# Kernel optimization log

Hardware: AMD Instinct MI355X
Metric: run time of the kernel (lower is better)

## Reference

```python
import jax, jax.numpy as jnp
import numpy as np

N, E, U, L = 10000, 320000, 256, 3


def setup_inputs() -> dict:
    key = jax.random.key(0)
    ks = jax.random.split(key, 16)
    s = 0.05
    p = {}
    p["pos"] = jax.random.normal(ks[0], (N, 2), jnp.float32)
    p["edge_attr_in"] = jax.random.uniform(ks[1], (E, 1), jnp.float32)
    p["edge_index"] = jax.random.randint(ks[2], (2, E), 0, N)
    p["Wp"] = jax.random.normal(ks[3], (2, U), jnp.float32) * s
    p["bp"] = jnp.zeros((U,), jnp.float32)
    p["Wa"] = jax.random.normal(ks[4], (1, U), jnp.float32) * s
    p["ba"] = jnp.zeros((U,), jnp.float32)
    p["W1"] = jax.random.normal(ks[5], (L, U, U), jnp.float32) * s
    p["b1"] = jnp.zeros((L, U), jnp.float32)
    p["W2"] = jax.random.normal(ks[6], (L, U, U), jnp.float32) * s
    p["b2"] = jnp.zeros((L, U), jnp.float32)
    p["We"] = jax.random.normal(ks[7], (L + 1, U, U), jnp.float32) * s
    p["be"] = jnp.zeros((L + 1, U), jnp.float32)
    p["Ws"] = jax.random.normal(ks[8], (L + 1, U, U), jnp.float32) * s
    p["Wt"] = jax.random.normal(ks[9], (L + 1, U, U), jnp.float32) * s
    p["Wm1"] = jax.random.normal(ks[10], (U + 1, U // 2), jnp.float32) * s
    p["bm1"] = jnp.zeros((U // 2,), jnp.float32)
    p["alpha"] = 0.25 * jnp.ones((1,), jnp.float32)  # PReLU default slope
    p["Wm2"] = jax.random.normal(ks[11], (U // 2, 1), jnp.float32) * s
    p["bm2"] = jnp.zeros((1,), jnp.float32)
    return p


def _forward(pos, edge_attr_in, edge_index, Wp, bp, Wa, ba, W1, b1, W2, b2,
             We, be, Ws, Wt, Wm1, bm1, alpha, Wm2, bm2):
    src, dst = edge_index[0], edge_index[1]
    x = pos @ Wp + bp                      # [N, U]
    e = edge_attr_in @ Wa + ba             # [E, U]

    def edge_update(x, e, l):
        # ResEdgeLinear: residual edge update from endpoint nodes + edge feats
        return e + jax.nn.relu(e @ We[l] + x[src] @ Ws[l] + x[dst] @ Wt[l] + be[l])

    for l in range(L):
        # ResNodeConv: gated gather-linear-scatter with residual
        gate = jax.nn.sigmoid(e)                                   # [E, U]
        msg = gate * (x[src] @ W2[l] + b2[l])                      # [E, U]
        agg = jax.ops.segment_sum(msg, dst, num_segments=N)        # [N, U]
        x_new = x + jax.nn.relu(x @ W1[l] + b1[l] + agg)
        e_new = edge_update(x, e, l)  # simultaneous update: both use old (x, e)
        x, e = x_new, e_new
    e = edge_update(x, e, L)

    h = jnp.concatenate([e, edge_attr_in[:, :1]], axis=-1) @ Wm1 + bm1
    h = jnp.where(h > 0, h, alpha * h)  # PReLU
    return h @ Wm2 + bm2                # [E, 1] logits


def reference(pos, edge_attr_in, edge_index, Wp, bp, Wa, ba, W1, b1, W2, b2,
              We, be, Ws, Wt, Wm1, bm1, alpha, Wm2, bm2):
    return _forward(pos, edge_attr_in, edge_index, Wp, bp, Wa, ba, W1, b1,
                    W2, b2, We, be, Ws, Wt, Wm1, bm1, alpha, Wm2, bm2)
```

## Files before the change

### kernel.cpp

```cpp
#include <hip/hip_runtime.h>
#include <stdint.h>

#define N_NODES 10000
#define N_EDGES 320000

using bf16x8 = __attribute__((ext_vector_type(8))) short;
using fp32x4 = __attribute__((ext_vector_type(4))) float;
using u16x8 = __attribute__((ext_vector_type(8))) unsigned short;
using i32x4 = __attribute__((ext_vector_type(4))) int;

__device__ __forceinline__ float bf2f(unsigned short u) {
  union { unsigned int i; float f; } v; v.i = ((unsigned int)u) << 16; return v.f;
}
__device__ __forceinline__ unsigned short f2bf(float f) {
  union { float f; unsigned int i; } v; v.f = f;
  unsigned int x = v.i;
  x += 0x7fffu + ((x >> 16) & 1u);
  return (unsigned short)(x >> 16);
}

#define A_POS 0
#define A_EA 20000
#define A_WP 340000
#define A_BP 340512
#define A_WA 340768
#define A_BA 341024
#define A_W1 341280
#define A_B1 537888
#define A_W2 538656
#define A_B2 735264
#define A_WE 736032
#define A_BE 998176
#define A_WS 999200
#define A_WT 1261344
#define A_WM1 1523488
#define A_BM1 1556384
#define A_AL 1556512
#define A_WM2 1556544
#define A_BM2 1556672
#define ARENA_USED 1556673
#define ARENA_TOT 1556736

__constant__ int g_off[19] = {A_POS, A_EA, A_WP, A_BP, A_WA, A_BA, A_W1, A_B1,
                              A_W2, A_B2, A_WE, A_BE, A_WS, A_WT, A_WM1,
                              A_BM1, A_AL, A_WM2, A_BM2};

struct Ptrs { const void* p[19]; };

__global__ void k_detect(const unsigned short* wpraw, int* flag, int* deg) {
  int i = blockIdx.x * 256 + threadIdx.x;
  if (i < N_NODES) deg[i] = 0;
  if (blockIdx.x == 0) {
    __shared__ int cnt;
    int tid = threadIdx.x;
    if (tid == 0) cnt = 0;
    __syncthreads();
    float v0 = bf2f(wpraw[tid]);
    float v1 = bf2f(wpraw[256 + tid]);
    int big = (fabsf(v0) > 100.f ? 1 : 0) + (fabsf(v1) > 100.f ? 1 : 0);
    atomicAdd(&cnt, big);
    __syncthreads();
    if (tid == 0) *flag = (cnt > 10) ? 1 : 0;
  }
}

__global__ void k_cast(Ptrs ptrs, const int* __restrict__ flag,
                       unsigned short* __restrict__ arena) {
  int a = blockIdx.x * 256 + threadIdx.x;
  if (a >= ARENA_USED) return;
  int z = 0;
#pragma unroll
  for (int j = 1; j < 19; ++j) if (a >= g_off[j]) z = j;
  int i = a - g_off[z];
  float v;
  if (*flag) v = ((const float*)ptrs.p[z])[i];
  else       v = bf2f(((const unsigned short*)ptrs.p[z])[i]);
  arena[a] = f2bf(v);
}

__global__ void k_prep(const unsigned short* __restrict__ arena,
                       unsigned short* nodeBT, unsigned short* WeT,
                       unsigned short* Wm1T, unsigned short* biascat) {
  int z = blockIdx.z;
  int i = blockIdx.x * 256 + threadIdx.x;
  if (z == 19) {
    if (i < 3072) {
      int l = i >> 10, j = i & 1023;
      unsigned short v = 0;
      if (j < 256) v = arena[A_B1 + l * 256 + j];
      else if (j < 512) v = arena[A_B2 + l * 256 + (j - 256)];
      biascat[i] = v;
    } else if (i < 3584) {
      biascat[i] = 0;
    }
    return;
  }
  const unsigned short* src; unsigned short* dst; int srcN = 256;
  if (z < 3)       {                 src = arena + A_W1 + z * 65536; dst = nodeBT + z * 262144; }
  else if (z < 6)  { int l = z - 3;  src = arena + A_W2 + l * 65536; dst = nodeBT + l * 262144 + 65536; }
  else if (z < 10) { int l = z - 6;  src = arena + A_WS + l * 65536;
                     dst = (l < 3) ? nodeBT + l * 262144 + 131072 : nodeBT + 786432; }
  else if (z < 14) { int l = z - 10; src = arena + A_WT + l * 65536;
                     dst = (l < 3) ? nodeBT + l * 262144 + 196608 : nodeBT + 786432 + 65536; }
  else if (z < 18) { int l = z - 14; src = arena + A_WE + l * 65536; dst = WeT + l * 65536; }
  else             { src = arena + A_WM1; dst = Wm1T; srcN = 128; }
  if (i < srcN * 256) {
    int k = i & 255, n = i >> 8;
    dst[i] = src[k * srcN + n];
  }
}

__global__ void k_pack(const unsigned short* __restrict__ src,
                       unsigned short* __restrict__ dst, int MT, int nchunks) {
  int c = blockIdx.x * 256 + threadIdx.x;
  if (c >= nchunks) return;
  int perg = MT * 512;
  int g = c / perg, r = c % perg;
  int ks = r / (64 * MT);
  int rem = r % (64 * MT);
  int mt = rem >> 6, lane = rem & 63;
  int q = lane >> 4, ll = lane & 15;
  int oc = g * (MT * 16) + (ll >> 2) * (MT * 4) + (ll & 3) + mt * 4;
  i32x4 v = *(const i32x4*)((const char*)src + ((long)oc << 9) + (ks << 6) + (q << 4));
  ((i32x4*)dst)[c] = v;
}

__global__ void k_init_x(const unsigned short* __restrict__ arena,
                         float* __restrict__ xf, unsigned short* __restrict__ xbf,
                         float* __restrict__ agg) {
  int n = blockIdx.x, c = threadIdx.x;
  float p0 = bf2f(arena[A_POS + 2 * n]), p1 = bf2f(arena[A_POS + 2 * n + 1]);
  float v = fmaf(p0, bf2f(arena[A_WP + c]),
                 fmaf(p1, bf2f(arena[A_WP + 256 + c]), bf2f(arena[A_BP + c])));
  long idx = ((long)n << 8) + c;
  xf[idx] = v;
  xbf[idx] = f2bf(v);
  agg[idx] = 0.f;
}

__global__ void k_hist(const int* __restrict__ dstA, int* __restrict__ deg) {
  int i = blockIdx.x * 256 + threadIdx.x;
  if (i < N_EDGES) {
    int d = dstA[i];
    if ((unsigned)d < N_NODES) atomicAdd(&deg[d], 1);
  }
}

__global__ void k_scan(const int* __restrict__ deg, int* __restrict__ rowptr,
                       int* __restrict__ cursor) {
  __shared__ int part[256];
  int tid = threadIdx.x;
  int base = tid * 40;
  int s = 0;
  for (int i = 0; i < 40; ++i) {
    int idx = base + i;
    if (idx < N_NODES) s += deg[idx];
  }
  part[tid] = s;
  __syncthreads();
  if (tid == 0) {
    int run = 0;
    for (int i = 0; i < 256; ++i) { int t = part[i]; part[i] = run; run += t; }
    rowptr[N_NODES] = run;
  }
  __syncthreads();
  int run = part[tid];
  for (int i = 0; i < 40; ++i) {
    int idx = base + i;
    if (idx < N_NODES) { rowptr[idx] = run; cursor[idx] = run; run += deg[idx]; }
  }
}

__global__ void k_fill(const int* __restrict__ dstA, const int* __restrict__ srcA,
                       const unsigned short* __restrict__ arena,
                       int* __restrict__ cursor, int* __restrict__ eid,
                       int* __restrict__ csrc, int* __restrict__ cdst,
                       unsigned short* __restrict__ eaC) {
  int i = blockIdx.x * 256 + threadIdx.x;
  if (i < N_EDGES) {
    int d = dstA[i]; if ((unsigned)d >= N_NODES) d = 0;
    int p = atomicAdd(&cursor[d], 1);
    if ((unsigned)p < N_EDGES) {
      eid[p] = i;
      int s = srcA[i]; if ((unsigned)s >= N_NODES) s = 0;
      csrc[p] = s;
      cdst[p] = d;
      eaC[p] = arena[A_EA + i];
    }
  }
}

#define SM_PITCH 528
#define XS_PITCH 144
#define EDGE_BLOCKS (N_EDGES / 128)

template <bool NT, int ROWS, int BLK>
__device__ __forceinline__ void stage_tile(char* smc, const unsigned short* src,
                                           long rowBase) {
  int tid = threadIdx.x;
#pragma unroll
  for (int it = 0; it < ROWS * 32 / BLK; ++it) {
    int lin = it * BLK + tid;
    int row = lin >> 5, g = lin & 31;
    const i32x4* p = (const i32x4*)((const char*)src + ((rowBase + row) << 9) + (g << 4));
    i32x4 v = NT ? __builtin_nontemporal_load(p) : *p;
    *(i32x4*)(smc + row * SM_PITCH + (g << 4)) = v;
  }
}

template <int MT, int NTT>
__device__ __forceinline__ void gemm_swap(const char* smc, const unsigned short* WTp,
                                          int colBase, fp32x4 (&acc)[MT][NTT]) {
  const int lane = threadIdx.x & 63;
  const int q = lane >> 4, ll = lane & 15;
  const char* wbase = (const char*)WTp + ((long)colBase << 9) + (lane << 4);
#pragma unroll
  for (int ks = 0; ks < 8; ++ks) {
    bf16x8 a[MT];
#pragma unroll
    for (int mt = 0; mt < MT; ++mt)
      a[mt] = *(const bf16x8*)(wbase + ((long)(ks * MT + mt) << 10));
    bf16x8 b[NTT];
#pragma unroll
    for (int nt = 0; nt < NTT; ++nt)
      b[nt] = *(const bf16x8*)(smc + (nt * 16 + ll) * SM_PITCH + (ks << 6) + (q << 4));
#pragma unroll
    for (int mt = 0; mt < MT; ++mt)
#pragma unroll
      for (int nt = 0; nt < NTT; ++nt)
        acc[mt][nt] = __builtin_amdgcn_mfma_f32_16x16x32_bf16(a[mt], b[nt], acc[mt][nt], 0, 0, 0);
  }
}

template <int NTT>
__device__ __forceinline__ void edge_epilogue_cx(
    char* smc, char* xsw, const fp32x4 (&acc)[4][NTT], const int* s_src,
    const int* s_dst, const unsigned short* XW, int xw_pitch, int xs_off,
    int xt_off, const unsigned short* bePtr, int colBase, int lane) {
  const int q = lane >> 4, ll = lane & 15;
  const int cb = colBase + q * 16;
  u16x8 be0 = *(const u16x8*)(bePtr + cb);
  u16x8 be1 = *(const u16x8*)(bePtr + cb + 8);
  const int prow = lane >> 3;
  const int ppc = lane & 7;
  const int pcol = xs_off + colBase + ppc * 8;
  u16x8 pfA = *(const u16x8*)(XW + (long)s_src[prow] * xw_pitch + pcol);
  u16x8 pfB = *(const u16x8*)(XW + (long)s_src[8 + prow] * xw_pitch + pcol);
#pragma unroll
  for (int nt = 0; nt < NTT; ++nt) {
    *(u16x8*)(xsw + prow * XS_PITCH + ppc * 16) = pfA;
    *(u16x8*)(xsw + (8 + prow) * XS_PITCH + ppc * 16) = pfB;
    if (nt + 1 < NTT) {
      int elA = (nt + 1) * 16 + prow;
      pfA = *(const u16x8*)(XW + (long)s_src[elA] * xw_pitch + pcol);
      pfB = *(const u16x8*)(XW + (long)s_src[elA + 8] * xw_pitch + pcol);
    }
    int el = nt * 16 + ll;
    int dn = s_dst[el];
    const unsigned short* xtrow = XW + (long)dn * xw_pitch + xt_off + cb;
    u16x8 xt0 = *(const u16x8*)(xtrow);
    u16x8 xt1 = *(const u16x8*)(xtrow + 8);
    u16x8 xs0 = *(const u16x8*)(xsw + ll * XS_PITCH + q * 32);
    u16x8 xs1 = *(const u16x8*)(xsw + ll * XS_PITCH + q * 32 + 16);
    u16x8* slot = (u16x8*)(smc + el * SM_PITCH + cb * 2);
    u16x8 er0 = slot[0], er1 = slot[1];
    u16x8 o0, o1;
#pragma unroll
    for (int mt = 0; mt < 4; ++mt)
#pragma unroll
      for (int r = 0; r < 4; ++r) {
        int i = mt * 4 + r;
        float xsv = bf2f(i < 8 ? xs0[i] : xs1[i - 8]);
        float xtv = bf2f(i < 8 ? xt0[i] : xt1[i - 8]);
        float erv = bf2f(i < 8 ? er0[i] : er1[i - 8]);
        float bev = bf2f(i < 8 ? be0[i] : be1[i - 8]);
        float v = acc[mt][nt][r] + xsv + xtv + bev;
        v = fmaxf(v, 0.f);
        unsigned short ob = f2bf(erv + v);
        if (i < 8) o0[i] = ob; else o1[i - 8] = ob;
      }
    slot[0] = o0;
    slot[1] = o1;
  }
}

template <int MODE>
__global__ __launch_bounds__(256, 2) void k_fat(
    unsigned short* __restrict__ e, const unsigned short* __restrict__ WT_edge,
    const unsigned short* __restrict__ XW_edge,
    const unsigned short* __restrict__ bePtr, const unsigned short* __restrict__ arena,
    const unsigned short* __restrict__ eaC,
    const int* __restrict__ csrc, const int* __restrict__ cdst,
    const unsigned short* __restrict__ xbf, const unsigned short* __restrict__ WT_node,
    const unsigned short* __restrict__ bias, unsigned short* __restrict__ XW_out) {
  __shared__ int4 sm4[128 * 33];
  __shared__ int4 xsb4[4 * 2304 / 16];
  __shared__ int s_src[128];
  __shared__ int s_dst[128];
  char* smc = (char*)sm4;
  const int tid = threadIdx.x;
  const int wave = tid >> 6, lane = tid & 63;
  const int q = lane >> 4, ll = lane & 15;

  if (blockIdx.x < EDGE_BLOCKS) {
    const long tileBase = (long)blockIdx.x * 128;
    const int colBase = wave * 64;
    if (MODE == 0) {
#pragma unroll
      for (int it = 0; it < 16; ++it) {
        int lin = it * 256 + tid;
        int row = lin >> 5, g = lin & 31;
        float eav = bf2f(eaC[tileBase + row]);
        int c0 = g * 8;
        bf16x8 ov;
#pragma unroll
        for (int j = 0; j < 8; ++j) {
          float f = fmaf(eav, bf2f(arena[A_WA + c0 + j]), bf2f(arena[A_BA + c0 + j]));
          ((unsigned short*)&ov)[j] = f2bf(f);
        }
        *(bf16x8*)(smc + row * SM_PITCH + (g << 4)) = ov;
      }
    } else {
      stage_tile<true, 128, 256>(smc, e, tileBase);
    }
    if (tid < 128) {
      long edge = tileBase + tid;
      int s = csrc[edge]; if ((unsigned)s >= N_NODES) s = 0;
      int d = cdst[edge]; if ((unsigned)d >= N_NODES) d = 0;
      s_src[tid] = s;
      s_dst[tid] = d;
    }
    __syncthreads();

    fp32x4 acc[4][8];
#pragma unroll
    for (int mt = 0; mt < 4; ++mt)
#pragma unroll
      for (int nt = 0; nt < 8; ++nt) acc[mt][nt] = 0.f;
    gemm_swap<4, 8>(smc, WT_edge, colBase, acc);
    __syncthreads();

    edge_epilogue_cx<8>(smc, (char*)xsb4 + wave * 2304, acc, s_src, s_dst,
                        XW_edge, 1024, 512, 768, bePtr, colBase, lane);
    __syncthreads();

#pragma unroll
    for (int it = 0; it < 16; ++it) {
      int lin = it * 256 + tid;
      int row = lin >> 5, g = lin & 31;
      i32x4 v = *(const i32x4*)(smc + row * SM_PITCH + (g << 4));
      __builtin_nontemporal_store(v, (i32x4*)((char*)e + ((tileBase + row) << 9) + (g << 4)));
    }
  } else {
    int b = blockIdx.x - EDGE_BLOCKS;
    int bx = b % 79, by = b / 79;
    const long tileBase = (long)bx * 128;
#pragma unroll
    for (int it = 0; it < 16; ++it) {
      int lin = it * 256 + tid;
      int row = lin >> 5, g = lin & 31;
      long rg = tileBase + row;
      if (rg > N_NODES - 1) rg = N_NODES - 1;
      i32x4 v = *(const i32x4*)((const char*)xbf + (rg << 9) + (g << 4));
      *(i32x4*)(smc + row * SM_PITCH + (g << 4)) = v;
    }
    __syncthreads();
    fp32x4 acc[2][8];
#pragma unroll
    for (int mt = 0; mt < 2; ++mt)
#pragma unroll
      for (int nt = 0; nt < 8; ++nt) acc[mt][nt] = 0.f;
    const int colBase = by * 128 + wave * 32;
    gemm_swap<2, 8>(smc, WT_node, colBase, acc);

    const int cb = colBase + q * 8;
    u16x8 bs8 = *(const u16x8*)(bias + cb);
#pragma unroll
    for (int nt = 0; nt < 8; ++nt) {
      long nn = tileBase + nt * 16 + ll;
      if (nn >= N_NODES) continue;
      u16x8 o0;
#pragma unroll
      for (int mt = 0; mt < 2; ++mt)
#pragma unroll
        for (int r = 0; r < 4; ++r) {
          int i = mt * 4 + r;
          o0[i] = f2bf(acc[mt][nt][r] + bf2f(bs8[i]));
        }
      *(u16x8*)(XW_out + nn * 1024 + cb) = o0;
    }
  }
}

__global__ __launch_bounds__(256, 2) void k_edge_last2(
    const unsigned short* __restrict__ e, const unsigned short* __restrict__ WeT2,
    const unsigned short* __restrict__ WeT3,
    const unsigned short* __restrict__ XW2, const unsigned short* __restrict__ XW3,
    const unsigned short* __restrict__ arena, const unsigned short* __restrict__ eaC,
    const int* __restrict__ csrc, const int* __restrict__ cdst,
    const unsigned short* __restrict__ Wm1T, const int* __restrict__ eid,
    const int* __restrict__ flag, void* __restrict__ out) {
  __shared__ int4 sm4[128 * 33];
  __shared__ int4 xsb4[4 * 2304 / 16];
  __shared__ int s_src[128];
  __shared__ int s_dst[128];
  char* smc = (char*)sm4;
  const long tileBase = (long)blockIdx.x * 128;
  const int tid = threadIdx.x;
  const int wave = tid >> 6, lane = tid & 63;
  const int q = lane >> 4, ll = lane & 15;
  const int colBase = wave * 64;
  char* xsw = (char*)xsb4 + wave * 2304;

  stage_tile<true, 128, 256>(smc, e, tileBase);
  if (tid < 128) {
    long edge = tileBase + tid;
    int s = csrc[edge]; if ((unsigned)s >= N_NODES) s = 0;
    int d = cdst[edge]; if ((unsigned)d >= N_NODES) d = 0;
    s_src[tid] = s;
    s_dst[tid] = d;
  }
  __syncthreads();

  fp32x4 acc[4][8];
#pragma unroll
  for (int mt = 0; mt < 4; ++mt)
#pragma unroll
    for (int nt = 0; nt < 8; ++nt) acc[mt][nt] = 0.f;
  gemm_swap<4, 8>(smc, WeT2, colBase, acc);
  __syncthreads();
  edge_epilogue_cx<8>(smc, xsw, acc, s_src, s_dst, XW2, 1024, 512, 768,
                      arena + A_BE + 2 * 256, colBase, lane);
  __syncthreads();

#pragma unroll
  for (int mt = 0; mt < 4; ++mt)
#pragma unroll
    for (int nt = 0; nt < 8; ++nt) acc[mt][nt] = 0.f;
  gemm_swap<4, 8>(smc, WeT3, colBase, acc);
  __syncthreads();
  edge_epilogue_cx<8>(smc, xsw, acc, s_src, s_dst, XW3, 512, 0, 256,
                      arena + A_BE + 3 * 256, colBase, lane);
  __syncthreads();

  fp32x4 acc2[2][8];
#pragma unroll
  for (int mt = 0; mt < 2; ++mt)
#pragma unroll
    for (int nt = 0; nt < 8; ++nt) acc2[mt][nt] = 0.f;
  const int colBase2 = wave * 32;
  gemm_swap<2, 8>(smc, Wm1T, colBase2, acc2);

  const int cb2 = colBase2 + q * 8;
  float alphaf = bf2f(arena[A_AL]);
  float bmc[8], wl[8], w2c[8];
#pragma unroll
  for (int i = 0; i < 8; ++i) {
    bmc[i] = bf2f(arena[A_BM1 + cb2 + i]);
    wl[i] = bf2f(arena[A_WM1 + 32768 + cb2 + i]);
    w2c[i] = bf2f(arena[A_WM2 + cb2 + i]);
  }
  __syncthreads();
  float* part = (float*)smc;
#pragma unroll
  for (int nt = 0; nt < 8; ++nt) {
    int el = nt * 16 + ll;
    float eav = bf2f(eaC[tileBase + el]);
    float ps = 0.f;
#pragma unroll
    for (int mt = 0; mt < 2; ++mt)
#pragma unroll
      for (int r = 0; r < 4; ++r) {
        int i = mt * 4 + r;
        float h = acc2[mt][nt][r] + bmc[i] + eav * wl[i];
        h = (h > 0.f) ? h : alphaf * h;
        ps += h * w2c[i];
      }
    ps += __shfl_xor(ps, 16, 64);
    ps += __shfl_xor(ps, 32, 64);
    if (q == 0) part[el * 4 + wave] = ps;
  }
  __syncthreads();
  if (tid < 128) {
    float t = part[tid * 4] + part[tid * 4 + 1] + part[tid * 4 + 2] + part[tid * 4 + 3]
            + bf2f(arena[A_BM2]);
    long row = tileBase + tid;
    int oe = eid[row]; if ((unsigned)oe >= N_EDGES) oe = 0;
    if (*flag) ((float*)out)[oe] = t;
    else       ((unsigned short*)out)[oe] = f2bf(t);
  }
}

__global__ __launch_bounds__(256, 2) void k_node_gemm(
    const unsigned short* __restrict__ xbf, const unsigned short* __restrict__ WT,
    const unsigned short* __restrict__ bias, unsigned short* __restrict__ out,
    int out_pitch) {
  __shared__ int4 sm4[128 * 33];
  char* smc = (char*)sm4;
  const long tileBase = (long)blockIdx.x * 128;
  {
    int tid = threadIdx.x;
#pragma unroll
    for (int it = 0; it < 16; ++it) {
      int lin = it * 256 + tid;
      int row = lin >> 5, g = lin & 31;
      long rg = tileBase + row;
      if (rg > N_NODES - 1) rg = N_NODES - 1;
      i32x4 v = *(const i32x4*)((const char*)xbf + (rg << 9) + (g << 4));
      *(i32x4*)(smc + row * SM_PITCH + (g << 4)) = v;
    }
  }
  __syncthreads();
  fp32x4 acc[2][8];
#pragma unroll
  for (int mt = 0; mt < 2; ++mt)
#pragma unroll
    for (int nt = 0; nt < 8; ++nt) acc[mt][nt] = 0.f;
  const int tid = threadIdx.x, wave = tid >> 6, lane = tid & 63;
  const int q = lane >> 4, ll = lane & 15;
  const int colBase = blockIdx.y * 128 + wave * 32;
  gemm_swap<2, 8>(smc, WT, colBase, acc);

  const int cb = colBase + q * 8;
  u16x8 bs8 = *(const u16x8*)(bias + cb);
#pragma unroll
  for (int nt = 0; nt < 8; ++nt) {
    long nn = tileBase + nt * 16 + ll;
    if (nn >= N_NODES) continue;
    u16x8 o0;
#pragma unroll
    for (int mt = 0; mt < 2; ++mt)
#pragma unroll
      for (int r = 0; r < 4; ++r) {
        int i = mt * 4 + r;
        o0[i] = f2bf(acc[mt][nt][r] + bf2f(bs8[i]));
      }
    *(u16x8*)(out + nn * out_pitch + cb) = o0;
  }
}

template <bool FIRST>
__global__ void k_agg(const int* __restrict__ csrc, const int* __restrict__ cdst,
                      const unsigned short* __restrict__ e,
                      const unsigned short* __restrict__ eaC,
                      const unsigned short* __restrict__ arena,
                      const unsigned short* __restrict__ XW, int xw_pitch, int x2_off,
                      float* __restrict__ agg) {
  __shared__ int s_src[64];
  __shared__ int s_dst[64];
  const long base = (long)blockIdx.x * 64;
  const int c = threadIdx.x;
  if (c < 64) {
    long r = base + c;
    int s = csrc[r]; if ((unsigned)s >= N_NODES) s = 0;
    int d = cdst[r]; if ((unsigned)d >= N_NODES) d = 0;
    s_src[c] = s;
    s_dst[c] = d;
  }
  __syncthreads();
  float wac = 0.f, bac = 0.f;
  if (FIRST) { wac = bf2f(arena[A_WA + c]); bac = bf2f(arena[A_BA + c]); }
  float a = 0.f;
  int run = s_dst[0];
  for (int b8 = 0; b8 < 64; b8 += 8) {
    float evv[8], x2v[8];
#pragma unroll
    for (int j = 0; j < 8; ++j) {
      int row = b8 + j;
      if (FIRST) evv[j] = fmaf(bf2f(eaC[base + row]), wac, bac);
      else evv[j] = bf2f(__builtin_nontemporal_load(e + ((base + row) << 8) + c));
      x2v[j] = bf2f(XW[(long)s_src[row] * xw_pitch + x2_off + c]);
    }
#pragma unroll
    for (int j = 0; j < 8; ++j) {
      int d = s_dst[b8 + j];
      if (d != run) {
        atomicAdd(&agg[((long)run << 8) + c], a);
        a = 0.f;
        run = d;
      }
      float gate = 1.f / (1.f + __expf(-evv[j]));
      a = fmaf(gate, x2v[j], a);
    }
  }
  atomicAdd(&agg[((long)run << 8) + c], a);
}

__global__ void k_node_update(float* __restrict__ xf, unsigned short* __restrict__ xbf,
                              const unsigned short* __restrict__ XW,
                              float* __restrict__ agg) {
  int n = blockIdx.x, c = threadIdx.x;
  long idx = ((long)n << 8) + c;
  float av = agg[idx];
  agg[idx] = 0.f;
  float t = bf2f(XW[((long)n << 10) + c]) + av;
  float nx = xf[idx] + fmaxf(t, 0.f);
  xf[idx] = nx;
  xbf[idx] = f2bf(nx);
}

extern "C" void kernel_launch(void* const* d_in, const int* in_sizes, int n_in,
                              void* d_out, int out_size, void* d_ws, size_t ws_size,
                              hipStream_t stream) {
  const int* eidx = (const int*)d_in[2];
  const int* srcA = eidx;
  const int* dstA = eidx + N_EDGES;
  (void)in_sizes; (void)n_in; (void)out_size;

  char* ws = (char*)d_ws;
  size_t off = 0;
  auto alloc = [&](size_t bytes) -> char* {
    char* p = ws + off;
    off = (off + bytes + 255) & ~(size_t)255;
    return p;
  };
  unsigned short* e_buf   = (unsigned short*)alloc((size_t)N_EDGES * 256 * 2);
  float*          xf      = (float*)alloc((size_t)N_NODES * 256 * 4);
  unsigned short* xbf     = (unsigned short*)alloc((size_t)N_NODES * 256 * 2);
  unsigned short* XWa     = (unsigned short*)alloc((size_t)N_NODES * 1024 * 2);
  unsigned short* XWb     = (unsigned short*)alloc((size_t)N_NODES * 1024 * 2);
  unsigned short* XW3     = (unsigned short*)alloc((size_t)N_NODES * 512 * 2);
  float*          agg     = (float*)alloc((size_t)N_NODES * 256 * 4);
  unsigned short* nodeBT  = (unsigned short*)alloc((size_t)917504 * 2);
  unsigned short* WeT     = (unsigned short*)alloc((size_t)4 * 65536 * 2);
  unsigned short* Wm1T    = (unsigned short*)alloc((size_t)32768 * 2);
  unsigned short* nodeBTp = (unsigned short*)alloc((size_t)917504 * 2);
  unsigned short* WeTp    = (unsigned short*)alloc((size_t)4 * 65536 * 2);
  unsigned short* Wm1Tp   = (unsigned short*)alloc((size_t)32768 * 2);
  unsigned short* biascat = (unsigned short*)alloc((size_t)3584 * 2);
  unsigned short* arena   = (unsigned short*)alloc((size_t)ARENA_TOT * 2);
  int* deg    = (int*)alloc((size_t)N_NODES * 4);
  int* rowptr = (int*)alloc((size_t)(N_NODES + 1) * 4);
  int* cursor = (int*)alloc((size_t)N_NODES * 4);
  int* eid    = (int*)alloc((size_t)N_EDGES * 4);
  int* csrc   = (int*)alloc((size_t)N_EDGES * 4);
  int* cdst   = (int*)alloc((size_t)N_EDGES * 4);
  unsigned short* eaC = (unsigned short*)alloc((size_t)N_EDGES * 2);
  int* flag   = (int*)alloc(4);
  if (ws_size < off) return;

  Ptrs ptrs;
  {
    int map[19] = {0, 1, 3, 4, 5, 6, 7, 8, 9, 10, 11, 12, 13, 14, 15, 16, 17, 18, 19};
    for (int j = 0; j < 19; ++j) ptrs.p[j] = d_in[map[j]];
  }

  dim3 blk(256);
  k_detect<<<dim3(40), blk, 0, stream>>>((const unsigned short*)d_in[3], flag, deg);
  k_cast<<<dim3((ARENA_USED + 255) / 256), blk, 0, stream>>>(ptrs, flag, arena);
  k_prep<<<dim3(256, 1, 20), blk, 0, stream>>>(arena, nodeBT, WeT, Wm1T, biascat);
  k_pack<<<dim3(448), blk, 0, stream>>>(nodeBT, nodeBTp, 2, 114688);
  k_pack<<<dim3(128), blk, 0, stream>>>(WeT, WeTp, 4, 32768);
  k_pack<<<dim3(16),  blk, 0, stream>>>(Wm1T, Wm1Tp, 2, 4096);
  k_init_x<<<dim3(N_NODES), blk, 0, stream>>>(arena, xf, xbf, agg);
  k_hist<<<dim3(N_EDGES / 256), blk, 0, stream>>>(dstA, deg);
  k_scan<<<dim3(1), blk, 0, stream>>>(deg, rowptr, cursor);
  k_fill<<<dim3(N_EDGES / 256), blk, 0, stream>>>(dstA, srcA, arena, cursor, eid, csrc,
                                                  cdst, eaC);

  k_node_gemm<<<dim3(79, 8), blk, 0, stream>>>(xbf, nodeBTp, biascat, XWa, 1024);
  k_agg<true><<<dim3(N_EDGES / 64), blk, 0, stream>>>(csrc, cdst, e_buf, eaC, arena,
                                                      XWa, 1024, 256, agg);
  k_node_update<<<dim3(N_NODES), blk, 0, stream>>>(xf, xbf, XWa, agg);
  k_fat<0><<<dim3(EDGE_BLOCKS + 632), blk, 0, stream>>>(
      e_buf, WeTp, XWa, arena + A_BE, arena, eaC, csrc, cdst,
      xbf, nodeBTp + 262144, biascat + 1024, XWb);
  k_agg<false><<<dim3(N_EDGES / 64), blk, 0, stream>>>(csrc, cdst, e_buf, eaC, arena,
                                                       XWb, 1024, 256, agg);
  k_node_update<<<dim3(N_NODES), blk, 0, stream>>>(xf, xbf, XWb, agg);
  k_fat<1><<<dim3(EDGE_BLOCKS + 632), blk, 0, stream>>>(
      e_buf, WeTp + 65536, XWb, arena + A_BE + 256, arena, eaC, csrc, cdst,
      xbf, nodeBTp + 2 * 262144, biascat + 2048, XWa);
  k_agg<false><<<dim3(N_EDGES / 64), blk, 0, stream>>>(csrc, cdst, e_buf, eaC, arena,
                                                       XWa, 1024, 256, agg);
  k_node_update<<<dim3(N_NODES), blk, 0, stream>>>(xf, xbf, XWa, agg);
  k_node_gemm<<<dim3(79, 4), blk, 0, stream>>>(xbf, nodeBTp + 786432, biascat + 3072, XW3, 512);
  k_edge_last2<<<dim3(EDGE_BLOCKS), blk, 0, stream>>>(
      e_buf, WeTp + 2 * 65536, WeTp + 3 * 65536, XWa, XW3, arena, eaC,
      csrc, cdst, Wm1Tp, eid, flag, d_out);
}
```

Baseline: 821.1 us.

## Prefetch source-node gathers before edge GEMM and software-pipeline dst gathers

Moves the gathered XW[src] row loads for all 8 column tiles ahead of the MFMA GEMM into registers, so their global latency overlaps the matrix multiply instead of stalling the epilogue. The XW[dst] gathers in the epilogue are now loaded one tile ahead. The shared-memory row pitch grows from 528 to 544 bytes to change the bank mapping. In exchange, the 16 extra u16x8 prefetch registers per thread raise register pressure under launch_bounds(256,2) and may cause spills or lower occupancy.

```diff
diff --git a/kernel.cpp b/kernel.cpp
--- a/kernel.cpp
+++ b/kernel.cpp
@@ -190,7 +190,7 @@
   }
 }
 
-#define SM_PITCH 528
+#define SM_PITCH 544
 #define XS_PITCH 144
 #define EDGE_BLOCKS (N_EDGES / 128)
 
@@ -233,33 +233,45 @@
 }
 
 template <int NTT>
+__device__ __forceinline__ void xs_prefetch(const int* s_src,
+                                            const unsigned short* XW, int xw_pitch,
+                                            int pcol, u16x8 (&pf0)[NTT],
+                                            u16x8 (&pf1)[NTT]) {
+  const int prow = (threadIdx.x & 63) >> 3;
+#pragma unroll
+  for (int nt = 0; nt < NTT; ++nt) {
+    pf0[nt] = *(const u16x8*)(XW + (long)s_src[nt * 16 + prow] * xw_pitch + pcol);
+    pf1[nt] = *(const u16x8*)(XW + (long)s_src[nt * 16 + 8 + prow] * xw_pitch + pcol);
+  }
+}
+
+template <int NTT>
 __device__ __forceinline__ void edge_epilogue_cx(
-    char* smc, char* xsw, const fp32x4 (&acc)[4][NTT], const int* s_src,
-    const int* s_dst, const unsigned short* XW, int xw_pitch, int xs_off,
-    int xt_off, const unsigned short* bePtr, int colBase, int lane) {
+    char* smc, char* xsw, const fp32x4 (&acc)[4][NTT],
+    const u16x8 (&pf0)[NTT], const u16x8 (&pf1)[NTT],
+    const int* s_dst, const unsigned short* XW, int xw_pitch, int xt_off,
+    const unsigned short* bePtr, int colBase, int lane) {
   const int q = lane >> 4, ll = lane & 15;
   const int cb = colBase + q * 16;
   u16x8 be0 = *(const u16x8*)(bePtr + cb);
   u16x8 be1 = *(const u16x8*)(bePtr + cb + 8);
   const int prow = lane >> 3;
   const int ppc = lane & 7;
-  const int pcol = xs_off + colBase + ppc * 8;
-  u16x8 pfA = *(const u16x8*)(XW + (long)s_src[prow] * xw_pitch + pcol);
-  u16x8 pfB = *(const u16x8*)(XW + (long)s_src[8 + prow] * xw_pitch + pcol);
+  const unsigned short* xtb = XW + xt_off + cb;
+  int dn0 = s_dst[ll];
+  u16x8 nxt0 = *(const u16x8*)(xtb + (long)dn0 * xw_pitch);
+  u16x8 nxt1 = *(const u16x8*)(xtb + (long)dn0 * xw_pitch + 8);
 #pragma unroll
   for (int nt = 0; nt < NTT; ++nt) {
-    *(u16x8*)(xsw + prow * XS_PITCH + ppc * 16) = pfA;
-    *(u16x8*)(xsw + (8 + prow) * XS_PITCH + ppc * 16) = pfB;
+    *(u16x8*)(xsw + prow * XS_PITCH + ppc * 16) = pf0[nt];
+    *(u16x8*)(xsw + (8 + prow) * XS_PITCH + ppc * 16) = pf1[nt];
+    u16x8 xt0 = nxt0, xt1 = nxt1;
     if (nt + 1 < NTT) {
-      int elA = (nt + 1) * 16 + prow;
-      pfA = *(const u16x8*)(XW + (long)s_src[elA] * xw_pitch + pcol);
-      pfB = *(const u16x8*)(XW + (long)s_src[elA + 8] * xw_pitch + pcol);
+      int dn2 = s_dst[(nt + 1) * 16 + ll];
+      nxt0 = *(const u16x8*)(xtb + (long)dn2 * xw_pitch);
+      nxt1 = *(const u16x8*)(xtb + (long)dn2 * xw_pitch + 8);
     }
     int el = nt * 16 + ll;
-    int dn = s_dst[el];
-    const unsigned short* xtrow = XW + (long)dn * xw_pitch + xt_off + cb;
-    u16x8 xt0 = *(const u16x8*)(xtrow);
-    u16x8 xt1 = *(const u16x8*)(xtrow + 8);
     u16x8 xs0 = *(const u16x8*)(xsw + ll * XS_PITCH + q * 32);
     u16x8 xs1 = *(const u16x8*)(xsw + ll * XS_PITCH + q * 32 + 16);
     u16x8* slot = (u16x8*)(smc + el * SM_PITCH + cb * 2);
@@ -293,7 +305,7 @@
     const int* __restrict__ csrc, const int* __restrict__ cdst,
     const unsigned short* __restrict__ xbf, const unsigned short* __restrict__ WT_node,
     const unsigned short* __restrict__ bias, unsigned short* __restrict__ XW_out) {
-  __shared__ int4 sm4[128 * 33];
+  __shared__ int4 sm4[128 * 34];
   __shared__ int4 xsb4[4 * 2304 / 16];
   __shared__ int s_src[128];
   __shared__ int s_dst[128];
@@ -332,6 +344,9 @@
     }
     __syncthreads();
 
+    u16x8 pf0[8], pf1[8];
+    xs_prefetch<8>(s_src, XW_edge, 1024, 512 + colBase + (lane & 7) * 8, pf0, pf1);
+
     fp32x4 acc[4][8];
 #pragma unroll
     for (int mt = 0; mt < 4; ++mt)
@@ -340,8 +355,8 @@
     gemm_swap<4, 8>(smc, WT_edge, colBase, acc);
     __syncthreads();
 
-    edge_epilogue_cx<8>(smc, (char*)xsb4 + wave * 2304, acc, s_src, s_dst,
-                        XW_edge, 1024, 512, 768, bePtr, colBase, lane);
+    edge_epilogue_cx<8>(smc, (char*)xsb4 + wave * 2304, acc, pf0, pf1, s_dst,
+                        XW_edge, 1024, 768, bePtr, colBase, lane);
     __syncthreads();
 
 #pragma unroll
@@ -400,7 +415,7 @@
     const int* __restrict__ csrc, const int* __restrict__ cdst,
     const unsigned short* __restrict__ Wm1T, const int* __restrict__ eid,
     const int* __restrict__ flag, void* __restrict__ out) {
-  __shared__ int4 sm4[128 * 33];
+  __shared__ int4 sm4[128 * 34];
   __shared__ int4 xsb4[4 * 2304 / 16];
   __shared__ int s_src[128];
   __shared__ int s_dst[128];
@@ -422,6 +437,8 @@
   }
   __syncthreads();
 
+  u16x8 pf0[8], pf1[8];
+  xs_prefetch<8>(s_src, XW2, 1024, 512 + colBase + (lane & 7) * 8, pf0, pf1);
   fp32x4 acc[4][8];
 #pragma unroll
   for (int mt = 0; mt < 4; ++mt)
@@ -429,17 +446,18 @@
     for (int nt = 0; nt < 8; ++nt) acc[mt][nt] = 0.f;
   gemm_swap<4, 8>(smc, WeT2, colBase, acc);
   __syncthreads();
-  edge_epilogue_cx<8>(smc, xsw, acc, s_src, s_dst, XW2, 1024, 512, 768,
+  edge_epilogue_cx<8>(smc, xsw, acc, pf0, pf1, s_dst, XW2, 1024, 768,
                       arena + A_BE + 2 * 256, colBase, lane);
   __syncthreads();
 
+  xs_prefetch<8>(s_src, XW3, 512, colBase + (lane & 7) * 8, pf0, pf1);
 #pragma unroll
   for (int mt = 0; mt < 4; ++mt)
 #pragma unroll
     for (int nt = 0; nt < 8; ++nt) acc[mt][nt] = 0.f;
   gemm_swap<4, 8>(smc, WeT3, colBase, acc);
   __syncthreads();
-  edge_epilogue_cx<8>(smc, xsw, acc, s_src, s_dst, XW3, 512, 0, 256,
+  edge_epilogue_cx<8>(smc, xsw, acc, pf0, pf1, s_dst, XW3, 512, 256,
                       arena + A_BE + 3 * 256, colBase, lane);
   __syncthreads();
 
@@ -495,7 +513,7 @@
     const unsigned short* __restrict__ xbf, const unsigned short* __restrict__ WT,
     const unsigned short* __restrict__ bias, unsigned short* __restrict__ out,
     int out_pitch) {
-  __shared__ int4 sm4[128 * 33];
+  __shared__ int4 sm4[128 * 34];
   char* smc = (char*)sm4;
   const long tileBase = (long)blockIdx.x * 128;
   {
```

Result: slower. 0.9999 ms (+21.8%).
